# Performance work log

Hardware: AMD Instinct MI355X
Metric: run time of the kernel (lower is better)

Reference implementation:

```python
import jax, jax.numpy as jnp
import numpy as np

B, T, I, H = 512, 2048, 13, 13


def setup_inputs() -> dict:
    key = jax.random.key(0)
    ks = jax.random.split(key, 7)
    s_in = 1.0 / np.sqrt(H)
    return {
        "x": jax.random.normal(ks[0], (B, T, I), dtype=jnp.float32),
        "W_ih": jax.random.uniform(ks[1], (4 * H, I), jnp.float32, -s_in, s_in),
        "W_hh": jax.random.uniform(ks[2], (4 * H, H), jnp.float32, -s_in, s_in),
        "b_ih": jax.random.uniform(ks[3], (4 * H,), jnp.float32, -s_in, s_in),
        "b_hh": jax.random.uniform(ks[4], (4 * H,), jnp.float32, -s_in, s_in),
        "fc_w": jax.random.uniform(ks[5], (1, H), jnp.float32, -s_in, s_in),
        "fc_b": jax.random.uniform(ks[6], (1,), jnp.float32, -s_in, s_in),
    }


def _lstm(x, W_ih, W_hh, b_ih, b_hh):
    # Precompute input-to-gate projections for all timesteps: [B, T, 4H]
    xg = jnp.einsum("bti,gi->btg", x, W_ih) + b_ih + b_hh
    xg = jnp.swapaxes(xg, 0, 1)  # [T, B, 4H] for scan
    h0 = jnp.zeros((x.shape[0], H), x.dtype)
    c0 = jnp.zeros((x.shape[0], H), x.dtype)

    def step(carry, xg_t):
        h, c = carry
        gates = xg_t + h @ W_hh.T  # [B, 4H]
        i_g, f_g, g_g, o_g = jnp.split(gates, 4, axis=-1)  # PyTorch order i,f,g,o
        i_g = jax.nn.sigmoid(i_g)
        f_g = jax.nn.sigmoid(f_g)
        g_g = jnp.tanh(g_g)
        o_g = jax.nn.sigmoid(o_g)
        c_new = f_g * c + i_g * g_g
        h_new = o_g * jnp.tanh(c_new)
        return (h_new, c_new), h_new

    _, hs = jax.lax.scan(step, (h0, c0), xg)  # hs: [T, B, H]
    return jnp.swapaxes(hs, 0, 1)  # [B, T, H]


def reference(x, W_ih, W_hh, b_ih, b_hh, fc_w, fc_b):
    out = _lstm(x, W_ih, W_hh, b_ih, b_hh)  # [B, T, H]
    out = jnp.einsum("bth,oh->bto", out, fc_w) + fc_b  # [B, T, 1]
    return jax.nn.sigmoid(out)
```

## Files before the change

kernel.cpp:

```cpp
#include <hip/hip_runtime.h>
#include <hip/hip_fp16.h>

#define BB 512
#define TT 2048

typedef _Float16 half2v __attribute__((ext_vector_type(2)));

__device__ __forceinline__ float fexp2(float x){ return __builtin_amdgcn_exp2f(x); }
__device__ __forceinline__ float frcp(float x){ return __builtin_amdgcn_rcpf(x); }
__device__ __forceinline__ float sigm(float x){ return frcp(1.f + fexp2(-1.4426950408889634f*x)); }
__device__ __forceinline__ float tanhfast(float x){ return 1.f - 2.f*frcp(1.f + fexp2(2.8853900817779268f*x)); }

#define QB(v, ctrl) __int_as_float(__builtin_amdgcn_mov_dpp(__float_as_int(v), (ctrl), 0xF, 0xF, true))
#define RL(v, l)    __builtin_amdgcn_readlane((v), (l))

__global__ __launch_bounds__(256) void k_xg2(const float* __restrict__ x,
                                             const float* __restrict__ Wih,
                                             const float* __restrict__ bih,
                                             const float* __restrict__ bhh,
                                             unsigned* __restrict__ xg_u)
{
  __shared__ float    xs[13*256];
  __shared__ unsigned ot[32*212];
  const int tid = threadIdx.x;
  const int b   = blockIdx.x >> 3;
  const int t0  = (blockIdx.x & 7) << 8;

  const float* xsrc = x + ((size_t)b*TT + t0)*13;
  #pragma unroll
  for (int it=0; it<13; ++it) xs[tid + it*256] = xsrc[tid + it*256];
  __syncthreads();

  float xv[13];
  #pragma unroll
  for (int k=0;k<13;k++) xv[k] = xs[tid*13+k];

  const int tgl = tid >> 3, u = tid & 7;
  unsigned short* otp = (unsigned short*)ot;
  #pragma unroll 2
  for (int g=0; g<52; ++g){
    float acc = bih[g] + bhh[g];
    #pragma unroll
    for (int k=0;k<13;k++) acc = fmaf(Wih[g*13+k], xv[k], acc);
    const float sc = (g>=26 && g<39) ? -2.8853900817779268f : -1.4426950408889634f;
    otp[tgl*424 + g*8 + u] = __half_as_ushort(__float2half(acc*sc));
  }
  __syncthreads();

  unsigned* dst = xg_u + ((((size_t)b*256 + (t0>>3))*416) >> 1);
  #pragma unroll
  for (int it=0; it<26; ++it){
    int i2  = tid + it*256;
    int us  = i2*2;
    int t2  = (int)((unsigned)us / 416u);
    int rem = us - t2*416;
    dst[i2] = ot[t2*212 + (rem>>1)];
  }
}

__global__ __launch_bounds__(64, 1) void k_rec4(const float* __restrict__ Whh,
                                                const unsigned short* __restrict__ xg,
                                                unsigned short* __restrict__ hs)
{
  const int lane = threadIdx.x;
  const int b    = blockIdx.x;
  const int q    = lane & 3;
  const int j    = lane >> 2;
  const int jc   = (j < 13) ? j : 12;
  const int e    = q*13 + jc;

  const float kq = (q==2) ? -2.8853900817779268f : -1.4426950408889634f;
  const float gm = (q==2) ? -5.7707801635558536f : 1.f;
  const float ga = (q==2) ?  2.8853900817779268f : 0.f;

  float w[13];
  #pragma unroll
  for (int k=0;k<13;k++) w[k] = Whh[e*13 + k]*kq;

  const char* gbase = (const char*)xg + ((size_t)b*256*416 + (size_t)e*8)*2;

  float h = 0.f, c_ = 0.f;
  float hb0=0,hb1=0,hb2=0,hb3=0,hb4=0,hb5=0,hb6=0,hb7=0,hb8=0,hb9=0,hb10=0,hb11=0,hb12=0;

  const bool wr = (q==0) && (j<13);
  uint4* hsrow = (uint4*)(hs + ((size_t)b*13 + jc)*TT);
  float hprev = 0.f;
  unsigned pk0=0u, pk1=0u, pk2=0u, pk3=0u;

#define STEP(xv_, u_) do {                                                    \
    float dA = fmaf(w[0], hb0, (xv_));                                        \
    dA = fmaf(w[1], hb1, dA);                                                 \
    dA = fmaf(w[2], hb2, dA);                                                 \
    dA = fmaf(w[3], hb3, dA);                                                 \
    dA = fmaf(w[4], hb4, dA);                                                 \
    float dB = w[5]*hb5;                                                      \
    dB = fmaf(w[6], hb6, dB);                                                 \
    dB = fmaf(w[7], hb7, dB);                                                 \
    dB = fmaf(w[8], hb8, dB);                                                 \
    float dC = w[9]*hb9;                                                      \
    dC = fmaf(w[10], hb10, dC);                                               \
    dC = fmaf(w[11], hb11, dC);                                               \
    dC = fmaf(w[12], hb12, dC);                                               \
    float s  = (dB + dC) + dA;                                                \
    float r  = frcp(1.f + fexp2(s));                                          \
    float g  = fmaf(gm, r, ga);                                               \
    float ggb = QB(g, 0xAA);                                                  \
    float gfb = QB(g, 0x55);                                                  \
    float gob = QB(g, 0xFF);                                                  \
    float go2 = gob + gob;                                                    \
    c_ = fmaf(gfb, c_, g*ggb);                                                \
    float r2 = frcp(1.f + fexp2(c_));                                         \
    h = fmaf(go2, r2, -gob);                                                  \
    if ((u_) & 1) {                                                           \
      unsigned pp = __builtin_bit_cast(unsigned,                              \
                      __builtin_amdgcn_cvt_pkrtz(hprev, h));                  \
      if ((u_)==1) pk0=pp; else if ((u_)==3) pk1=pp;                          \
      else if ((u_)==5) pk2=pp; else pk3=pp;                                  \
    } else hprev = h;                                                         \
    int hv_ = __float_as_int(h);                                              \
    hb0  = __int_as_float(RL(hv_, 0));                                        \
    hb1  = __int_as_float(RL(hv_, 4));                                        \
    hb2  = __int_as_float(RL(hv_, 8));                                        \
    hb3  = __int_as_float(RL(hv_, 12));                                       \
    hb4  = __int_as_float(RL(hv_, 16));                                       \
    hb5  = __int_as_float(RL(hv_, 20));                                       \
    hb6  = __int_as_float(RL(hv_, 24));                                       \
    hb7  = __int_as_float(RL(hv_, 28));                                       \
    hb8  = __int_as_float(RL(hv_, 32));                                       \
    hb9  = __int_as_float(RL(hv_, 36));                                       \
    hb10 = __int_as_float(RL(hv_, 40));                                       \
    hb11 = __int_as_float(RL(hv_, 44));                                       \
    hb12 = __int_as_float(RL(hv_, 48));                                       \
  } while(0)

#define XLO(w_) (float)(__builtin_bit_cast(half2v, (w_)).x)
#define XHI(w_) (float)(__builtin_bit_cast(half2v, (w_)).y)

#define STEP8(Q) do {                                                         \
    STEP(XLO(Q.x), 0); STEP(XHI(Q.x), 1);                                     \
    STEP(XLO(Q.y), 2); STEP(XHI(Q.y), 3);                                     \
    STEP(XLO(Q.z), 4); STEP(XHI(Q.z), 5);                                     \
    STEP(XLO(Q.w), 6); STEP(XHI(Q.w), 7);                                     \
    if (wr) *hsrow = make_uint4(pk0, pk1, pk2, pk3);                          \
    ++hsrow;                                                                  \
  } while(0)

  uint4 q0 = *(const uint4*)(gbase);
  uint4 q1 = *(const uint4*)(gbase + 832);
  uint4 q2 = *(const uint4*)(gbase + 2*832);
  uint4 q3 = *(const uint4*)(gbase + 3*832);

  for (int i=0; i<63; ++i){
    const char* pn = gbase + (size_t)(4*i+4)*832;
    uint4 c0 = q0; q0 = *(const uint4*)(pn);
    STEP8(c0);
    uint4 c1 = q1; q1 = *(const uint4*)(pn + 832);
    STEP8(c1);
    uint4 c2 = q2; q2 = *(const uint4*)(pn + 2*832);
    STEP8(c2);
    uint4 c3 = q3; q3 = *(const uint4*)(pn + 3*832);
    STEP8(c3);
  }
  STEP8(q0); STEP8(q1); STEP8(q2); STEP8(q3);

#undef STEP8
#undef STEP
#undef XLO
#undef XHI
}

__global__ __launch_bounds__(256) void k_out2(const unsigned short* __restrict__ hs,
                                              const float* __restrict__ fcw,
                                              const float* __restrict__ fcb,
                                              float* __restrict__ out)
{
  int idx = blockIdx.x*256 + threadIdx.x;
  int b   = idx >> 11;
  int t   = idx & 2047;
  const unsigned short* row = hs + (size_t)b*13*TT + t;
  float acc = fcb[0];
  #pragma unroll
  for (int j=0;j<13;j++){
    float hj = (float)__builtin_bit_cast(_Float16, row[(size_t)j*TT]);
    acc = fmaf(fcw[j], hj, acc);
  }
  out[idx] = sigm(acc);
}

__global__ __launch_bounds__(64) void k_rec_fb(
    const float* __restrict__ x,   const float* __restrict__ Whh,
    const float* __restrict__ Wih, const float* __restrict__ bih, const float* __restrict__ bhh,
    const float* __restrict__ fcw, const float* __restrict__ fcb,
    float* __restrict__ out)
{
  const int lane = threadIdx.x;
  const int c    = lane >> 4;
  const int j    = lane & 15;
  const int b    = blockIdx.x*4 + c;
  const bool act = (j < 13);
  const int jj   = act ? j : 0;

  float whh[4][13], wih[4][13], bias[4];
  #pragma unroll
  for (int q=0;q<4;q++){
    #pragma unroll
    for (int k=0;k<13;k++){
      float w1 = Whh[(q*13+jj)*13 + k];
      float w2 = Wih[(q*13+jj)*13 + k];
      whh[q][k] = act ? w1 : 0.f;
      wih[q][k] = act ? w2 : 0.f;
    }
    bias[q] = bih[q*13+jj] + bhh[q*13+jj];
  }
  const float fcwj = act ? fcw[jj] : 0.f;
  const float fcb0 = fcb[0];

  const float* xpf = x + (size_t)b*(TT*13) + jj;
  float* op = out + (size_t)b*TT;

  float h = 0.f, cs = 0.f;
  float xsc = *xpf;

  for (int t=0; t<TT; ++t){
    float xscn = 0.f;
    if (t+1 < TT) { xpf += 13; xscn = *xpf; }

    float hb[13], xb[13];
    {
      int hbits = __float_as_int(h);
      int xbits = __float_as_int(xsc);
      #define HB(k) hb[k] = __int_as_float(__builtin_amdgcn_ds_swizzle(hbits, ((k)<<5)|0x10)); \
                    xb[k] = __int_as_float(__builtin_amdgcn_ds_swizzle(xbits, ((k)<<5)|0x10));
      HB(0) HB(1) HB(2) HB(3) HB(4) HB(5) HB(6) HB(7) HB(8) HB(9) HB(10) HB(11) HB(12)
      #undef HB
    }
    float a0 = bias[0], a1 = bias[1], a2 = bias[2], a3 = bias[3];
    #pragma unroll
    for (int k=0;k<13;k++){
      float xk = xb[k], hk = hb[k];
      a0 += wih[0][k]*xk + whh[0][k]*hk;
      a1 += wih[1][k]*xk + whh[1][k]*hk;
      a2 += wih[2][k]*xk + whh[2][k]*hk;
      a3 += wih[3][k]*xk + whh[3][k]*hk;
    }
    float ig = sigm(a0), fg = sigm(a1), gg = tanhfast(a2), og = sigm(a3);
    cs = fg*cs + ig*gg;
    h  = og * tanhfast(cs);

    float p = act ? fcwj*h : 0.f;
    #define RED(m) p += __int_as_float(__builtin_amdgcn_ds_swizzle(__float_as_int(p), ((m)<<10)|0x1F));
    RED(1) RED(2) RED(4) RED(8)
    #undef RED
    if (j == 0) op[t] = sigm(p + fcb0);
    xsc = xscn;
  }
}

extern "C" void kernel_launch(void* const* d_in, const int* in_sizes, int n_in,
                              void* d_out, int out_size, void* d_ws, size_t ws_size,
                              hipStream_t stream)
{
  const float* x   = (const float*)d_in[0];
  const float* Wih = (const float*)d_in[1];
  const float* Whh = (const float*)d_in[2];
  const float* bih = (const float*)d_in[3];
  const float* bhh = (const float*)d_in[4];
  const float* fcw = (const float*)d_in[5];
  const float* fcb = (const float*)d_in[6];
  float* out = (float*)d_out;

  const size_t XG_BYTES = (size_t)BB*256*416*2;
  const size_t HS_BYTES = (size_t)BB*13*TT*2;

  if (ws_size >= XG_BYTES + HS_BYTES){
    unsigned*       xg = (unsigned*)d_ws;
    unsigned short* hs = (unsigned short*)((char*)d_ws + XG_BYTES);
    k_xg2<<<dim3(BB*8), dim3(256), 0, stream>>>(x, Wih, bih, bhh, xg);
    k_rec4<<<dim3(BB), dim3(64), 0, stream>>>(Whh, (const unsigned short*)xg, hs);
    k_out2<<<dim3((BB*TT)/256), dim3(256), 0, stream>>>(hs, fcw, fcb, out);
  } else {
    k_rec_fb<<<dim3(BB/4), dim3(64), 0, stream>>>(x, Whh, Wih, bih, bhh, fcw, fcb, out);
  }
}
```

Baseline: 339.3 us.

## Fuse input projection into recurrent kernel and use fp16 dot2 for hidden matvec

Removes the separate input-projection kernel and computes the xg projections inside each recurrent block before the scan, writing them to that block's own workspace slice. The recurrent matvec now uses packed fp16 weights and hidden states with fdot2, which cuts per-step FMAs and readlanes from 13 to 7 by packing pairs of h via DPP. The gate math is reordered to broadcast raw sigmoid outputs. The recurrent state is held in fp16 for the matvec, which costs precision, and the serial pre-pass uses only 512 single-wave blocks, so it may be slower than the old parallel projection kernel.

```diff
diff --git a/kernel.cpp b/kernel.cpp
--- a/kernel.cpp
+++ b/kernel.cpp
@@ -14,52 +14,25 @@
 #define QB(v, ctrl) __int_as_float(__builtin_amdgcn_mov_dpp(__float_as_int(v), (ctrl), 0xF, 0xF, true))
 #define RL(v, l)    __builtin_amdgcn_readlane((v), (l))
 
-__global__ __launch_bounds__(256) void k_xg2(const float* __restrict__ x,
-                                             const float* __restrict__ Wih,
-                                             const float* __restrict__ bih,
-                                             const float* __restrict__ bhh,
-                                             unsigned* __restrict__ xg_u)
-{
-  __shared__ float    xs[13*256];
-  __shared__ unsigned ot[32*212];
-  const int tid = threadIdx.x;
-  const int b   = blockIdx.x >> 3;
-  const int t0  = (blockIdx.x & 7) << 8;
-
-  const float* xsrc = x + ((size_t)b*TT + t0)*13;
-  #pragma unroll
-  for (int it=0; it<13; ++it) xs[tid + it*256] = xsrc[tid + it*256];
-  __syncthreads();
-
-  float xv[13];
-  #pragma unroll
-  for (int k=0;k<13;k++) xv[k] = xs[tid*13+k];
-
-  const int tgl = tid >> 3, u = tid & 7;
-  unsigned short* otp = (unsigned short*)ot;
-  #pragma unroll 2
-  for (int g=0; g<52; ++g){
-    float acc = bih[g] + bhh[g];
-    #pragma unroll
-    for (int k=0;k<13;k++) acc = fmaf(Wih[g*13+k], xv[k], acc);
-    const float sc = (g>=26 && g<39) ? -2.8853900817779268f : -1.4426950408889634f;
-    otp[tgl*424 + g*8 + u] = __half_as_ushort(__float2half(acc*sc));
-  }
-  __syncthreads();
-
-  unsigned* dst = xg_u + ((((size_t)b*256 + (t0>>3))*416) >> 1);
-  #pragma unroll
-  for (int it=0; it<26; ++it){
-    int i2  = tid + it*256;
-    int us  = i2*2;
-    int t2  = (int)((unsigned)us / 416u);
-    int rem = us - t2*416;
-    dst[i2] = ot[t2*212 + (rem>>1)];
-  }
-}
-
-__global__ __launch_bounds__(64, 1) void k_rec4(const float* __restrict__ Whh,
-                                                const unsigned short* __restrict__ xg,
+__device__ __forceinline__ unsigned pkrtz_u(float a, float b){
+  return __builtin_bit_cast(unsigned, __builtin_amdgcn_cvt_pkrtz(a, b));
+}
+
+__device__ __forceinline__ float fdot2(half2v a, half2v b, float c){
+#if __has_builtin(__builtin_amdgcn_fdot2)
+  return __builtin_amdgcn_fdot2(a, b, c, false);
+#else
+  float r = fmaf((float)a.x, (float)b.x, c);
+  return fmaf((float)a.y, (float)b.y, r);
+#endif
+}
+
+__global__ __launch_bounds__(64, 1) void k_rec5(const float* __restrict__ x,
+                                                const float* __restrict__ Wih,
+                                                const float* __restrict__ Whh,
+                                                const float* __restrict__ bih,
+                                                const float* __restrict__ bhh,
+                                                unsigned short* __restrict__ xg,
                                                 unsigned short* __restrict__ hs)
 {
   const int lane = threadIdx.x;
@@ -70,67 +43,82 @@
   const int e    = q*13 + jc;
 
   const float kq = (q==2) ? -2.8853900817779268f : -1.4426950408889634f;
-  const float gm = (q==2) ? -5.7707801635558536f : 1.f;
-  const float ga = (q==2) ?  2.8853900817779268f : 0.f;
-
-  float w[13];
-  #pragma unroll
-  for (int k=0;k<13;k++) w[k] = Whh[e*13 + k]*kq;
-
-  const char* gbase = (const char*)xg + ((size_t)b*256*416 + (size_t)e*8)*2;
+
+  unsigned wp[7];
+  {
+    float wt[14];
+    #pragma unroll
+    for (int k=0;k<13;k++) wt[k] = Whh[e*13 + k]*kq;
+    wt[13] = 0.f;
+    #pragma unroll
+    for (int m=0;m<7;m++) wp[m] = pkrtz_u(wt[2*m], wt[2*m+1]);
+  }
+
+  char* xgb = (char*)xg + (size_t)b*256*832;
+
+  {
+    const float* xrow = x + (size_t)b*TT*13;
+    for (int chunk=0; chunk<32; ++chunk){
+      const int t = (chunk<<6) + lane;
+      const float* p = xrow + t*13;
+      float xv[13];
+      #pragma unroll
+      for (int k=0;k<13;k++) xv[k] = p[k];
+      unsigned short* ob = (unsigned short*)(xgb + (size_t)(t>>3)*832) + (t&7);
+      #pragma unroll 4
+      for (int g=0; g<52; ++g){
+        float acc = bih[g] + bhh[g];
+        #pragma unroll
+        for (int k=0;k<13;k++) acc = fmaf(Wih[g*13+k], xv[k], acc);
+        acc *= (g>=26 && g<39) ? -2.8853900817779268f : -1.4426950408889634f;
+        ob[g*8] = __half_as_ushort(__float2half(acc));
+      }
+    }
+    __builtin_amdgcn_s_waitcnt(0);
+    __threadfence_block();
+  }
+
+  const char* gbase = (const char*)xgb + (size_t)e*16;
 
   float h = 0.f, c_ = 0.f;
-  float hb0=0,hb1=0,hb2=0,hb3=0,hb4=0,hb5=0,hb6=0,hb7=0,hb8=0,hb9=0,hb10=0,hb11=0,hb12=0;
+  int hp0=0,hp1=0,hp2=0,hp3=0,hp4=0,hp5=0,hp6=0;
 
   const bool wr = (q==0) && (j<13);
   uint4* hsrow = (uint4*)(hs + ((size_t)b*13 + jc)*TT);
   float hprev = 0.f;
   unsigned pk0=0u, pk1=0u, pk2=0u, pk3=0u;
 
+#define H2(v_) __builtin_bit_cast(half2v, (unsigned)(v_))
+
 #define STEP(xv_, u_) do {                                                    \
-    float dA = fmaf(w[0], hb0, (xv_));                                        \
-    dA = fmaf(w[1], hb1, dA);                                                 \
-    dA = fmaf(w[2], hb2, dA);                                                 \
-    dA = fmaf(w[3], hb3, dA);                                                 \
-    dA = fmaf(w[4], hb4, dA);                                                 \
-    float dB = w[5]*hb5;                                                      \
-    dB = fmaf(w[6], hb6, dB);                                                 \
-    dB = fmaf(w[7], hb7, dB);                                                 \
-    dB = fmaf(w[8], hb8, dB);                                                 \
-    float dC = w[9]*hb9;                                                      \
-    dC = fmaf(w[10], hb10, dC);                                               \
-    dC = fmaf(w[11], hb11, dC);                                               \
-    dC = fmaf(w[12], hb12, dC);                                               \
-    float s  = (dB + dC) + dA;                                                \
+    float dA = fdot2(H2(wp[0]), H2(hp0), (xv_));                              \
+    dA = fdot2(H2(wp[1]), H2(hp1), dA);                                       \
+    dA = fdot2(H2(wp[2]), H2(hp2), dA);                                       \
+    dA = fdot2(H2(wp[3]), H2(hp3), dA);                                       \
+    float dB = fdot2(H2(wp[4]), H2(hp4), 0.f);                                \
+    dB = fdot2(H2(wp[5]), H2(hp5), dB);                                       \
+    dB = fdot2(H2(wp[6]), H2(hp6), dB);                                       \
+    float s  = dA + dB;                                                       \
     float r  = frcp(1.f + fexp2(s));                                          \
-    float g  = fmaf(gm, r, ga);                                               \
-    float ggb = QB(g, 0xAA);                                                  \
-    float gfb = QB(g, 0x55);                                                  \
-    float gob = QB(g, 0xFF);                                                  \
+    float gfb = QB(r, 0x55);                                                  \
+    float gtb = QB(r, 0xAA);                                                  \
+    float gob = QB(r, 0xFF);                                                  \
+    float ggb = fmaf(-5.7707801635558536f, gtb, 2.8853900817779268f);         \
+    c_ = fmaf(gfb, c_, r*ggb);                                                \
+    float r2 = frcp(1.f + fexp2(c_));                                         \
     float go2 = gob + gob;                                                    \
-    c_ = fmaf(gfb, c_, g*ggb);                                                \
-    float r2 = frcp(1.f + fexp2(c_));                                         \
     h = fmaf(go2, r2, -gob);                                                  \
     if ((u_) & 1) {                                                           \
-      unsigned pp = __builtin_bit_cast(unsigned,                              \
-                      __builtin_amdgcn_cvt_pkrtz(hprev, h));                  \
+      unsigned pp = pkrtz_u(hprev, h);                                        \
       if ((u_)==1) pk0=pp; else if ((u_)==3) pk1=pp;                          \
       else if ((u_)==5) pk2=pp; else pk3=pp;                                  \
     } else hprev = h;                                                         \
-    int hv_ = __float_as_int(h);                                              \
-    hb0  = __int_as_float(RL(hv_, 0));                                        \
-    hb1  = __int_as_float(RL(hv_, 4));                                        \
-    hb2  = __int_as_float(RL(hv_, 8));                                        \
-    hb3  = __int_as_float(RL(hv_, 12));                                       \
-    hb4  = __int_as_float(RL(hv_, 16));                                       \
-    hb5  = __int_as_float(RL(hv_, 20));                                       \
-    hb6  = __int_as_float(RL(hv_, 24));                                       \
-    hb7  = __int_as_float(RL(hv_, 28));                                       \
-    hb8  = __int_as_float(RL(hv_, 32));                                       \
-    hb9  = __int_as_float(RL(hv_, 36));                                       \
-    hb10 = __int_as_float(RL(hv_, 40));                                       \
-    hb11 = __int_as_float(RL(hv_, 44));                                       \
-    hb12 = __int_as_float(RL(hv_, 48));                                       \
+    float hnb = __int_as_float(__builtin_amdgcn_mov_dpp(__float_as_int(h),    \
+                                 0x104, 0xF, 0xF, true));      \
+    int pki = (int)pkrtz_u(h, hnb);                                           \
+    hp0 = RL(pki, 0);  hp1 = RL(pki, 8);  hp2 = RL(pki, 16);                  \
+    hp3 = RL(pki, 24); hp4 = RL(pki, 32); hp5 = RL(pki, 40);                  \
+    hp6 = RL(pki, 48);                                                        \
   } while(0)
 
 #define XLO(w_) (float)(__builtin_bit_cast(half2v, (w_)).x)
@@ -167,6 +155,7 @@
 #undef STEP
 #undef XLO
 #undef XHI
+#undef H2
 }
 
 __global__ __launch_bounds__(256) void k_out2(const unsigned short* __restrict__ hs,
@@ -269,14 +258,13 @@
   const float* fcb = (const float*)d_in[6];
   float* out = (float*)d_out;
 
-  const size_t XG_BYTES = (size_t)BB*256*416*2;
+  const size_t XG_BYTES = (size_t)BB*256*832;
   const size_t HS_BYTES = (size_t)BB*13*TT*2;
 
   if (ws_size >= XG_BYTES + HS_BYTES){
-    unsigned*       xg = (unsigned*)d_ws;
+    unsigned short* xg = (unsigned short*)d_ws;
     unsigned short* hs = (unsigned short*)((char*)d_ws + XG_BYTES);
-    k_xg2<<<dim3(BB*8), dim3(256), 0, stream>>>(x, Wih, bih, bhh, xg);
-    k_rec4<<<dim3(BB), dim3(64), 0, stream>>>(Whh, (const unsigned short*)xg, hs);
+    k_rec5<<<dim3(BB), dim3(64), 0, stream>>>(x, Wih, Whh, bih, bhh, xg, hs);
     k_out2<<<dim3((BB*TT)/256), dim3(256), 0, stream>>>(hs, fcw, fcb, out);
   } else {
     k_rec_fb<<<dim3(BB/4), dim3(64), 0, stream>>>(x, Whh, Wih, bih, bhh, fcw, fcb, out);
```

Result: slower. 429.9 us (+26.7%).

## Fuse output projection into recurrent kernel via spare lane 52

Applied to the files above, without the earlier changes.

Removes the separate output kernel and the fp16 hidden-state buffer. Lane 52, previously idle, now computes the fc projection plus sigmoid with the same dot-product path as the gates. Its fc bias is packed into the precomputed xg stream as a 53rd gate slot, and its result is lagged one step because it uses the previous h. This drops a launch and the hs write and read traffic. In exchange the xg row stride grows and the recurrent kernel does extra capture and store work each step.

```diff
diff --git a/kernel.cpp b/kernel.cpp
--- a/kernel.cpp
+++ b/kernel.cpp
@@ -14,10 +14,11 @@
 #define QB(v, ctrl) __int_as_float(__builtin_amdgcn_mov_dpp(__float_as_int(v), (ctrl), 0xF, 0xF, true))
 #define RL(v, l)    __builtin_amdgcn_readlane((v), (l))
 
-__global__ __launch_bounds__(256) void k_xg2(const float* __restrict__ x,
+__global__ __launch_bounds__(256) void k_xg3(const float* __restrict__ x,
                                              const float* __restrict__ Wih,
                                              const float* __restrict__ bih,
                                              const float* __restrict__ bhh,
+                                             const float* __restrict__ fcb,
                                              unsigned* __restrict__ xg_u)
 {
   __shared__ float    xs[13*256];
@@ -45,47 +46,67 @@
     const float sc = (g>=26 && g<39) ? -2.8853900817779268f : -1.4426950408889634f;
     otp[tgl*424 + g*8 + u] = __half_as_ushort(__float2half(acc*sc));
   }
+  otp[tgl*424 + 52*8 + u] =
+      __half_as_ushort(__float2half(-1.4426950408889634f * fcb[0]));
   __syncthreads();
 
-  unsigned* dst = xg_u + ((((size_t)b*256 + (t0>>3))*416) >> 1);
-  #pragma unroll
-  for (int it=0; it<26; ++it){
-    int i2  = tid + it*256;
-    int us  = i2*2;
-    int t2  = (int)((unsigned)us / 416u);
-    int rem = us - t2*416;
-    dst[i2] = ot[t2*212 + (rem>>1)];
+  unsigned* dst = xg_u + (size_t)b*(256*212) + (size_t)(blockIdx.x & 7)*(32*212);
+  #pragma unroll
+  for (int it=0; it<27; ++it){
+    int i2 = tid + it*256;
+    if (i2 < 32*212) dst[i2] = ot[i2];
   }
 }
 
-__global__ __launch_bounds__(64, 1) void k_rec4(const float* __restrict__ Whh,
+__global__ __launch_bounds__(64, 1) void k_rec7(const float* __restrict__ Whh,
+                                                const float* __restrict__ fcw,
+                                                const float* __restrict__ fcb,
                                                 const unsigned short* __restrict__ xg,
-                                                unsigned short* __restrict__ hs)
+                                                float* __restrict__ out)
 {
   const int lane = threadIdx.x;
   const int b    = blockIdx.x;
   const int q    = lane & 3;
   const int j    = lane >> 2;
   const int jc   = (j < 13) ? j : 12;
-  const int e    = q*13 + jc;
+  const int e    = (lane == 52) ? 52 : q*13 + jc;
 
   const float kq = (q==2) ? -2.8853900817779268f : -1.4426950408889634f;
   const float gm = (q==2) ? -5.7707801635558536f : 1.f;
   const float ga = (q==2) ?  2.8853900817779268f : 0.f;
-
+  const float fcbias = -1.4426950408889634f * fcb[0];
+
+  const float* wsrc = (lane == 52) ? fcw : (Whh + e*13);
   float w[13];
   #pragma unroll
-  for (int k=0;k<13;k++) w[k] = Whh[e*13 + k]*kq;
-
-  const char* gbase = (const char*)xg + ((size_t)b*256*416 + (size_t)e*8)*2;
+  for (int k=0;k<13;k++) w[k] = wsrc[k]*kq;
+
+  const char* gbase = (const char*)xg + (size_t)b*(256*848) + (size_t)e*16;
 
   float h = 0.f, c_ = 0.f;
   float hb0=0,hb1=0,hb2=0,hb3=0,hb4=0,hb5=0,hb6=0,hb7=0,hb8=0,hb9=0,hb10=0,hb11=0,hb12=0;
 
-  const bool wr = (q==0) && (j<13);
-  uint4* hsrow = (uint4*)(hs + ((size_t)b*13 + jc)*TT);
-  float hprev = 0.f;
-  unsigned pk0=0u, pk1=0u, pk2=0u, pk3=0u;
+  float p0=0,p1=0,p2=0,p3=0,p4=0,p5=0,p6=0,p7=0;
+  float* op = out + (size_t)b*TT;
+  bool first = true;
+
+#define CAPTURE(gv_, u_) do {                                                 \
+    if ((u_)==1) p0=(gv_); else if ((u_)==2) p1=(gv_);                        \
+    else if ((u_)==3) p2=(gv_); else if ((u_)==4) p3=(gv_);                   \
+    else if ((u_)==5) p4=(gv_); else if ((u_)==6) p5=(gv_);                   \
+    else if ((u_)==7) p6=(gv_);                                               \
+    else { p7=(gv_);                                                          \
+      if (!first){                                                            \
+        if (lane == 52){                                                      \
+          float4* o4 = (float4*)op;                                           \
+          o4[0] = make_float4(p0,p1,p2,p3);                                   \
+          o4[1] = make_float4(p4,p5,p6,p7);                                   \
+        }                                                                     \
+        op += 8;                                                              \
+      }                                                                       \
+      first = false;                                                          \
+    }                                                                         \
+  } while(0)
 
 #define STEP(xv_, u_) do {                                                    \
     float dA = fmaf(w[0], hb0, (xv_));                                        \
@@ -104,6 +125,7 @@
     float s  = (dB + dC) + dA;                                                \
     float r  = frcp(1.f + fexp2(s));                                          \
     float g  = fmaf(gm, r, ga);                                               \
+    CAPTURE(g, u_);                                                           \
     float ggb = QB(g, 0xAA);                                                  \
     float gfb = QB(g, 0x55);                                                  \
     float gob = QB(g, 0xFF);                                                  \
@@ -111,12 +133,6 @@
     c_ = fmaf(gfb, c_, g*ggb);                                                \
     float r2 = frcp(1.f + fexp2(c_));                                         \
     h = fmaf(go2, r2, -gob);                                                  \
-    if ((u_) & 1) {                                                           \
-      unsigned pp = __builtin_bit_cast(unsigned,                              \
-                      __builtin_amdgcn_cvt_pkrtz(hprev, h));                  \
-      if ((u_)==1) pk0=pp; else if ((u_)==3) pk1=pp;                          \
-      else if ((u_)==5) pk2=pp; else pk3=pp;                                  \
-    } else hprev = h;                                                         \
     int hv_ = __float_as_int(h);                                              \
     hb0  = __int_as_float(RL(hv_, 0));                                        \
     hb1  = __int_as_float(RL(hv_, 4));                                        \
@@ -141,50 +157,54 @@
     STEP(XLO(Q.y), 2); STEP(XHI(Q.y), 3);                                     \
     STEP(XLO(Q.z), 4); STEP(XHI(Q.z), 5);                                     \
     STEP(XLO(Q.w), 6); STEP(XHI(Q.w), 7);                                     \
-    if (wr) *hsrow = make_uint4(pk0, pk1, pk2, pk3);                          \
-    ++hsrow;                                                                  \
   } while(0)
 
   uint4 q0 = *(const uint4*)(gbase);
-  uint4 q1 = *(const uint4*)(gbase + 832);
-  uint4 q2 = *(const uint4*)(gbase + 2*832);
-  uint4 q3 = *(const uint4*)(gbase + 3*832);
+  uint4 q1 = *(const uint4*)(gbase + 848);
+  uint4 q2 = *(const uint4*)(gbase + 2*848);
+  uint4 q3 = *(const uint4*)(gbase + 3*848);
 
   for (int i=0; i<63; ++i){
-    const char* pn = gbase + (size_t)(4*i+4)*832;
+    const char* pn = gbase + (size_t)(4*i+4)*848;
     uint4 c0 = q0; q0 = *(const uint4*)(pn);
     STEP8(c0);
-    uint4 c1 = q1; q1 = *(const uint4*)(pn + 832);
+    uint4 c1 = q1; q1 = *(const uint4*)(pn + 848);
     STEP8(c1);
-    uint4 c2 = q2; q2 = *(const uint4*)(pn + 2*832);
+    uint4 c2 = q2; q2 = *(const uint4*)(pn + 2*848);
     STEP8(c2);
-    uint4 c3 = q3; q3 = *(const uint4*)(pn + 3*832);
+    uint4 c3 = q3; q3 = *(const uint4*)(pn + 3*848);
     STEP8(c3);
   }
   STEP8(q0); STEP8(q1); STEP8(q2); STEP8(q3);
+
+  {
+    float s = fcbias;
+    s = fmaf(w[0],  hb0,  s);
+    s = fmaf(w[1],  hb1,  s);
+    s = fmaf(w[2],  hb2,  s);
+    s = fmaf(w[3],  hb3,  s);
+    s = fmaf(w[4],  hb4,  s);
+    s = fmaf(w[5],  hb5,  s);
+    s = fmaf(w[6],  hb6,  s);
+    s = fmaf(w[7],  hb7,  s);
+    s = fmaf(w[8],  hb8,  s);
+    s = fmaf(w[9],  hb9,  s);
+    s = fmaf(w[10], hb10, s);
+    s = fmaf(w[11], hb11, s);
+    s = fmaf(w[12], hb12, s);
+    float r = frcp(1.f + fexp2(s));
+    if (lane == 52){
+      float4* o4 = (float4*)op;
+      o4[0] = make_float4(p0,p1,p2,p3);
+      o4[1] = make_float4(p4,p5,p6,r);
+    }
+  }
 
 #undef STEP8
 #undef STEP
+#undef CAPTURE
 #undef XLO
 #undef XHI
-}
-
-__global__ __launch_bounds__(256) void k_out2(const unsigned short* __restrict__ hs,
-                                              const float* __restrict__ fcw,
-                                              const float* __restrict__ fcb,
-                                              float* __restrict__ out)
-{
-  int idx = blockIdx.x*256 + threadIdx.x;
-  int b   = idx >> 11;
-  int t   = idx & 2047;
-  const unsigned short* row = hs + (size_t)b*13*TT + t;
-  float acc = fcb[0];
-  #pragma unroll
-  for (int j=0;j<13;j++){
-    float hj = (float)__builtin_bit_cast(_Float16, row[(size_t)j*TT]);
-    acc = fmaf(fcw[j], hj, acc);
-  }
-  out[idx] = sigm(acc);
 }
 
 __global__ __launch_bounds__(64) void k_rec_fb(
@@ -269,15 +289,13 @@
   const float* fcb = (const float*)d_in[6];
   float* out = (float*)d_out;
 
-  const size_t XG_BYTES = (size_t)BB*256*416*2;
-  const size_t HS_BYTES = (size_t)BB*13*TT*2;
-
-  if (ws_size >= XG_BYTES + HS_BYTES){
-    unsigned*       xg = (unsigned*)d_ws;
-    unsigned short* hs = (unsigned short*)((char*)d_ws + XG_BYTES);
-    k_xg2<<<dim3(BB*8), dim3(256), 0, stream>>>(x, Wih, bih, bhh, xg);
-    k_rec4<<<dim3(BB), dim3(64), 0, stream>>>(Whh, (const unsigned short*)xg, hs);
-    k_out2<<<dim3((BB*TT)/256), dim3(256), 0, stream>>>(hs, fcw, fcb, out);
+  const size_t XG_BYTES = (size_t)BB*256*848;
+
+  if (ws_size >= XG_BYTES){
+    unsigned* xg = (unsigned*)d_ws;
+    k_xg3<<<dim3(BB*8), dim3(256), 0, stream>>>(x, Wih, bih, bhh, fcb, xg);
+    k_rec7<<<dim3(BB), dim3(64), 0, stream>>>(Whh, fcw, fcb,
+                                              (const unsigned short*)xg, out);
   } else {
     k_rec_fb<<<dim3(BB/4), dim3(64), 0, stream>>>(x, Whh, Wih, bih, bhh, fcw, fcb, out);
   }
```

Measured after the change: 323.9 us. 1.05x faster.
